# Kernel optimization log

Hardware: AMD Instinct MI355X
Metric: run time of the kernel (lower is better)

Reference implementation:

```python
import jax, jax.numpy as jnp
import numpy as np

CHUNK = 128
EPS = 1e-12


def causal_prod(q, k, v, chunk=CHUNK):
    """Chunk-parallel causal linear attention numerator and denominator.
    q,k: [B,H,S,D]; v: [B,H,S,E].
    Returns N: [B,H,S,E] = q_n . cumsum_{m<=n}(k_m v_m^T)
            D: [B,H,S]   = q_n . cumsum_{m<=n} k_m
    """
    B, H, S, D = q.shape
    E = v.shape[-1]
    nc = S // chunk
    # [nc, B, H, C, D]
    qc = q.reshape(B, H, nc, chunk, D).transpose(2, 0, 1, 3, 4)
    kc = k.reshape(B, H, nc, chunk, D).transpose(2, 0, 1, 3, 4)
    vc = v.reshape(B, H, nc, chunk, E).transpose(2, 0, 1, 3, 4)
    mask = jnp.tril(jnp.ones((chunk, chunk), dtype=bool))  # j <= i

    def step(carry, xs):
        S_state, Z_state = carry  # [B,H,D,E], [B,H,D]
        qb, kb, vb = xs           # [B,H,C,D], [B,H,C,D], [B,H,C,E]
        scores = jnp.einsum('bhid,bhjd->bhij', qb, kb)
        scores = jnp.where(mask, scores, 0.0)
        # intra-chunk causal part + inter-chunk state part
        Nb = jnp.einsum('bhij,bhje->bhie', scores, vb) \
             + jnp.einsum('bhid,bhde->bhie', qb, S_state)
        Db = scores.sum(-1) + jnp.einsum('bhid,bhd->bhi', qb, Z_state)
        S_state = S_state + jnp.einsum('bhjd,bhje->bhde', kb, vb)
        Z_state = Z_state + kb.sum(axis=2)
        return (S_state, Z_state), (Nb, Db)

    init = (jnp.zeros((B, H, D, E), q.dtype), jnp.zeros((B, H, D), q.dtype))
    _, (N, Dv) = jax.lax.scan(step, init, (qc, kc, vc))
    N = N.transpose(1, 2, 0, 3, 4).reshape(B, H, S, E)
    Dv = Dv.transpose(1, 2, 0, 3).reshape(B, H, S)
    return N, Dv


def setup_inputs() -> dict:
    key = jax.random.key(0)
    k0, k1, k2, k3, k4 = jax.random.split(key, 5)
    B, H, S, D = 2, 8, 4096, 64
    # feature-mapped q/k are positive (softmax random features) -> uniform
    q = jax.random.uniform(k0, (B, H, S, D), dtype=jnp.float32)
    k = jax.random.uniform(k1, (B, H, S, D), dtype=jnp.float32)
    q_rot = jax.random.uniform(k2, (B, H, S, D), dtype=jnp.float32)
    k_rot = jax.random.uniform(k3, (B, H, S, D), dtype=jnp.float32)
    v = jax.random.normal(k4, (B, H, S, D), dtype=jnp.float32)
    return {"q": q, "k": k, "q_rot": q_rot, "k_rot": k_rot, "v": v, "horizon": 512}


def reference(q, k, q_rot, k_rot, v, horizon):
    # causal_linear_attention with local=horizon, rotary branch active
    N1, D1 = causal_prod(q, k, v)
    N2, D2 = causal_prod(q_rot, k_rot, v)
    N = N1 + N2
    Dd = D1 + D2
    local = horizon
    # subtract contribution of keys older than the local window
    ql = q[:, :, local:]
    kl = k[:, :, :-local]
    vl = v[:, :, :-local]
    qrl = q_rot[:, :, local:]
    krl = k_rot[:, :, :-local]
    Ns1, Ds1 = causal_prod(ql, kl, vl)
    Ns2, Ds2 = causal_prod(qrl, krl, vl)
    N = N.at[:, :, local:].add(-(Ns1 + Ns2))
    Dd = Dd.at[:, :, local:].add(-(Ds1 + Ds2))
    out = N * (1.0 / (Dd + EPS))[..., None]
    return out
```

## Files before the change

### kernel.cpp

```cpp
#include <hip/hip_runtime.h>

#define S_LEN 4096
#define Dh 64
#define KC_TILE 16384
#define VT_TILE 8192

typedef __attribute__((ext_vector_type(8))) short bf16x8;
typedef __attribute__((ext_vector_type(4))) short bf16x4;
typedef __attribute__((ext_vector_type(4))) float f32x4;
typedef __attribute__((ext_vector_type(16))) float f32x16;
typedef __attribute__((ext_vector_type(4))) unsigned u32x4;

__device__ __forceinline__ short f2bf(float f) {
    union { float f; unsigned u; } c; c.f = f;
    unsigned u = c.u + 0x7FFFu + ((c.u >> 16) & 1u);
    return (short)(u >> 16);
}

__device__ __forceinline__ unsigned cvt_pk(float lo, float hi) {
    unsigned r;
    asm("v_cvt_pk_bf16_f32 %0, %1, %2" : "=v"(r) : "v"(lo), "v"(hi));
    return r;
}

__device__ __forceinline__ void pl32swap(unsigned& a, unsigned& b) {
    asm("v_permlane32_swap_b32 %0, %1" : "+v"(a), "+v"(b));
}

__global__ __launch_bounds__(256) void prepack2(
    const float* __restrict__ k, const float* __restrict__ kr,
    const float* __restrict__ v, char* __restrict__ ws,
    unsigned long long vt_base, int k_slots)
{
    const int t = blockIdx.x * 256 + threadIdx.x;
    if (t < k_slots) {
        const int bh = t >> 16;
        const int r = t & 65535;
        const int tile = r >> 10;
        const int s = r & 1023;
        const int l = s & 63;
        const int c = s >> 6;
        const int fs = c >> 1, half = c & 1;
        const int key = half * 32 + (l & 31);
        const int f0 = fs * 16 + (l >> 5) * 8;
        const size_t row = ((size_t)bh * S_LEN + tile * 64 + key) * Dh;
        const float* src = (f0 < 64) ? (k + row + f0) : (kr + row + f0 - 64);
        f32x4 a = *(const f32x4*)src;
        f32x4 b = *(const f32x4*)(src + 4);
        u32x4 w;
        w[0] = cvt_pk(a[0], a[1]); w[1] = cvt_pk(a[2], a[3]);
        w[2] = cvt_pk(b[0], b[1]); w[3] = cvt_pk(b[2], b[3]);
        *(u32x4*)(ws + (size_t)(bh * 64 + tile) * KC_TILE + s * 16) = w;
    } else {
        const int t2 = t - k_slots;
        const int bh = t2 >> 15;
        const int r = t2 & 32767;
        const int tile = r >> 9;
        const int s = r & 511;
        const int l = s & 63;
        const int c = s >> 6;
        const int kb = c >> 2, ks = (c >> 1) & 1, eh = c & 1;
        const int e = eh * 32 + (l & 31);
        const int key0 = kb * 32 + ks * 16 + (l >> 5) * 8;
        const float* src = v + ((size_t)bh * S_LEN + tile * 64 + key0) * Dh + e;
        float x0 = src[0],      x1 = src[Dh],     x2 = src[2 * Dh], x3 = src[3 * Dh];
        float x4 = src[4 * Dh], x5 = src[5 * Dh], x6 = src[6 * Dh], x7 = src[7 * Dh];
        u32x4 w;
        w[0] = cvt_pk(x0, x1); w[1] = cvt_pk(x2, x3);
        w[2] = cvt_pk(x4, x5); w[3] = cvt_pk(x6, x7);
        *(u32x4*)(ws + vt_base + (size_t)(bh * 64 + tile) * VT_TILE + s * 16) = w;
    }
}

__global__ __launch_bounds__(64, 3) void swin_attn5(
    const float* __restrict__ q, const float* __restrict__ qr,
    const char* __restrict__ ws, unsigned long long vt_base,
    const int* __restrict__ hor, float* __restrict__ out)
{
    const int W = hor[0];
    const int nwg = gridDim.x;
    const int cpx = nwg >> 3;
    const int bid = blockIdx.x;
    const int wg = (bid & 7) * cpx + (bid >> 3);
    const int bh = wg >> 7;
    const int q0 = (wg & 127) * 32;
    const size_t base = (size_t)bh * S_LEN * Dh;

    const int lane = threadIdx.x;
    const int hi = lane >> 5;
    const int l32 = lane & 31;

    __shared__ float sD[32];

    const int qg = q0 + l32;

    bf16x8 qf[8];
    {
        const float* qrow  = q  + base + (size_t)qg * Dh;
        const float* qrrow = qr + base + (size_t)qg * Dh;
        #pragma unroll
        for (int fs = 0; fs < 8; ++fs) {
            int feat = fs * 16 + hi * 8;
            const float* src = (feat < 64) ? (qrow + feat) : (qrrow + feat - 64);
            f32x4 a = *(const f32x4*)src;
            f32x4 b = *(const f32x4*)(src + 4);
            u32x4 w;
            w[0] = cvt_pk(a[0], a[1]); w[1] = cvt_pk(a[2], a[3]);
            w[2] = cvt_pk(b[0], b[1]); w[3] = cvt_pk(b[2], b[3]);
            qf[fs] = __builtin_bit_cast(bf16x8, w);
        }
    }

    f32x16 nacc0 = {};
    f32x16 nacc1 = {};
    float dsum = 0.f;

    const int lo_q = q0 - W + 1;
    const int h_lo = (lo_q <= 0) ? 0 : (lo_q >> 5);
    const int h_hi = (q0 + 31) >> 5;

    const char* Kc = ws + (size_t)(bh << 6) * KC_TILE + lane * 16;
    const char* Vt = ws + vt_base + (size_t)(bh << 6) * VT_TILE + lane * 16;

#define KADDR(H, FS) (Kc + (size_t)((H) >> 1) * KC_TILE + ((((FS) << 1) + ((H) & 1)) << 10))
#define VADDR(H, C)  (Vt + (size_t)((H) >> 1) * VT_TILE + (((((H) & 1) << 2) + (C)) << 10))

    bf16x8 kf[8];
    bf16x8 vf[4];
    #pragma unroll
    for (int fs = 0; fs < 8; ++fs) kf[fs] = *(const bf16x8*)KADDR(h_lo, fs);
    #pragma unroll
    for (int c = 0; c < 4; ++c)    vf[c] = *(const bf16x8*)VADDR(h_lo, c);

    for (int h = h_lo; h <= h_hi; ++h) {
        const int hn = (h < h_hi) ? h + 1 : h;
        const int k0h = h << 5;

        f32x16 sac = {};
        __builtin_amdgcn_s_setprio(1);
        #pragma unroll
        for (int fs = 0; fs < 8; ++fs)
            sac = __builtin_amdgcn_mfma_f32_32x32x16_bf16(kf[fs], qf[fs], sac, 0, 0, 0);
        __builtin_amdgcn_s_setprio(0);

        #pragma unroll
        for (int fs = 0; fs < 8; ++fs) kf[fs] = *(const bf16x8*)KADDR(hn, fs);

        const bool dense = (k0h + 31 <= q0) && (k0h >= q0 + 32 - W);
        if (!dense) {
            #pragma unroll
            for (int r = 0; r < 16; ++r) {
                int key = k0h + (r & 3) + 8 * (r >> 2) + 4 * hi;
                if ((unsigned)(qg - key) >= (unsigned)W) sac[r] = 0.f;
            }
        }
        #pragma unroll
        for (int r = 0; r < 16; ++r) dsum += sac[r];

        unsigned w0 = cvt_pk(sac[0],  sac[1]);
        unsigned w1 = cvt_pk(sac[2],  sac[3]);
        unsigned w2 = cvt_pk(sac[4],  sac[5]);
        unsigned w3 = cvt_pk(sac[6],  sac[7]);
        unsigned w4 = cvt_pk(sac[8],  sac[9]);
        unsigned w5 = cvt_pk(sac[10], sac[11]);
        unsigned w6 = cvt_pk(sac[12], sac[13]);
        unsigned w7 = cvt_pk(sac[14], sac[15]);
        pl32swap(w0, w2);
        pl32swap(w1, w3);
        pl32swap(w4, w6);
        pl32swap(w5, w7);
        u32x4 p0v = {w0, w1, w2, w3};
        u32x4 p1v = {w4, w5, w6, w7};
        bf16x8 pa0 = __builtin_bit_cast(bf16x8, p0v);
        bf16x8 pa1 = __builtin_bit_cast(bf16x8, p1v);

        __builtin_amdgcn_s_setprio(1);
        nacc0 = __builtin_amdgcn_mfma_f32_32x32x16_bf16(pa0, vf[0], nacc0, 0, 0, 0);
        nacc1 = __builtin_amdgcn_mfma_f32_32x32x16_bf16(pa0, vf[1], nacc1, 0, 0, 0);
        nacc0 = __builtin_amdgcn_mfma_f32_32x32x16_bf16(pa1, vf[2], nacc0, 0, 0, 0);
        nacc1 = __builtin_amdgcn_mfma_f32_32x32x16_bf16(pa1, vf[3], nacc1, 0, 0, 0);
        __builtin_amdgcn_s_setprio(0);

        #pragma unroll
        for (int c = 0; c < 4; ++c) vf[c] = *(const bf16x8*)VADDR(hn, c);
    }
#undef KADDR
#undef VADDR

    unsigned da = __builtin_bit_cast(unsigned, dsum);
    unsigned db = da;
    pl32swap(da, db);
    float dfull = __builtin_bit_cast(float, da) + __builtin_bit_cast(float, db);
    float rcq = 1.0f / (dfull + 1e-12f);
    if (lane < 32) sD[l32] = rcq;
    __syncthreads();
    float rcv[16];
    #pragma unroll
    for (int r = 0; r < 16; ++r)
        rcv[r] = sD[(r & 3) + 8 * (r >> 2) + 4 * hi];

    #pragma unroll
    for (int r = 0; r < 16; ++r) {
        const int qrow = q0 + (r & 3) + 8 * (r >> 2) + 4 * hi;
        float* o = out + base + (size_t)qrow * Dh + l32;
        o[0]  = nacc0[r] * rcv[r];
        o[32] = nacc1[r] * rcv[r];
    }
}

__global__ __launch_bounds__(256, 2) void swin_attn_fb(
    const float* __restrict__ q, const float* __restrict__ k,
    const float* __restrict__ qr, const float* __restrict__ kr,
    const float* __restrict__ v, const int* __restrict__ hor,
    float* __restrict__ out)
{
    const int W = hor[0];
    const int q0 = blockIdx.x * 128;
    const int bh = blockIdx.y;
    const size_t base = (size_t)bh * S_LEN * Dh;

    const int tid = threadIdx.x;
    const int lane = tid & 63;
    const int wv = tid >> 6;
    const int g = lane >> 4;
    const int l16 = lane & 15;

    __shared__ __align__(16) char sK[64 * 256];
    __shared__ __align__(16) char sV[64 * 128];
    __shared__ __align__(16) char sS[4][32 * 128];

    bf16x8 qf[2][4];
    #pragma unroll
    for (int rb = 0; rb < 2; ++rb) {
        int qg = q0 + wv * 32 + rb * 16 + l16;
        const float* qrow  = q  + base + (size_t)qg * Dh;
        const float* qrrow = qr + base + (size_t)qg * Dh;
        #pragma unroll
        for (int fb = 0; fb < 4; ++fb) {
            int feat = fb * 32 + g * 8;
            const float* src = (feat < 64) ? (qrow + feat) : (qrrow + (feat - 64));
            f32x4 a = *(const f32x4*)src;
            f32x4 b = *(const f32x4*)(src + 4);
            bf16x8 fr;
            #pragma unroll
            for (int j = 0; j < 4; ++j) { fr[j] = f2bf(a[j]); fr[4 + j] = f2bf(b[j]); }
            qf[rb][fb] = fr;
        }
    }

    f32x4 nacc[2][4];
    f32x4 dacc[2];
    #pragma unroll
    for (int rb = 0; rb < 2; ++rb) {
        dacc[rb] = (f32x4){0.f, 0.f, 0.f, 0.f};
        #pragma unroll
        for (int eb = 0; eb < 4; ++eb) nacc[rb][eb] = (f32x4){0.f, 0.f, 0.f, 0.f};
    }
    bf16x8 ones;
    #pragma unroll
    for (int j = 0; j < 8; ++j) ones[j] = (short)0x3F80;

    const int lo_key = q0 - (W - 1);
    const int kt_lo = (lo_key <= 0) ? 0 : (lo_key >> 6);
    const int kt_hi = (q0 + 127) >> 6;

    for (int kt = kt_lo; kt <= kt_hi; ++kt) {
        const int k0 = kt << 6;
        __syncthreads();
        #pragma unroll
        for (int i = 0; i < 4; ++i) {
            int c = tid + 256 * i;
            int row = c >> 4;
            int f0 = (c & 15) * 8;
            const float* src = (f0 < 64) ? (k  + base + (size_t)(k0 + row) * Dh + f0)
                                         : (kr + base + (size_t)(k0 + row) * Dh + (f0 - 64));
            f32x4 a = *(const f32x4*)src;
            f32x4 b = *(const f32x4*)(src + 4);
            bf16x8 w8;
            #pragma unroll
            for (int j = 0; j < 4; ++j) { w8[j] = f2bf(a[j]); w8[4 + j] = f2bf(b[j]); }
            int off = row * 256 + ((f0 * 2) ^ ((row & 7) << 4));
            *(bf16x8*)(sK + off) = w8;
        }
        #pragma unroll
        for (int i = 0; i < 4; ++i) {
            int c = tid + 256 * i;
            int e = c & 63;
            int k4 = c >> 6;
            const float* src = v + base + (size_t)(k0 + k4 * 4) * Dh + e;
            bf16x4 w4;
            w4[0] = f2bf(src[0]); w4[1] = f2bf(src[Dh]);
            w4[2] = f2bf(src[2 * Dh]); w4[3] = f2bf(src[3 * Dh]);
            int off = e * 128 + ((k4 * 8) ^ ((e & 7) << 4));
            *(bf16x4*)(sV + off) = w4;
        }
        __syncthreads();

        const bool dense = (k0 + 63 <= q0) && (k0 >= q0 + 128 - W);
        #pragma unroll
        for (int kb = 0; kb < 4; ++kb) {
            bf16x8 kf[4];
            const int key = kb * 16 + l16;
            const int rowoff = key * 256;
            const int sw = (key & 7) << 4;
            #pragma unroll
            for (int fb = 0; fb < 4; ++fb)
                kf[fb] = *(const bf16x8*)(sK + rowoff + ((fb * 64 + g * 16) ^ sw));
            #pragma unroll
            for (int rb = 0; rb < 2; ++rb) {
                f32x4 s = {0.f, 0.f, 0.f, 0.f};
                #pragma unroll
                for (int fb = 0; fb < 4; ++fb)
                    s = __builtin_amdgcn_mfma_f32_16x16x32_bf16(qf[rb][fb], kf[fb], s, 0, 0, 0);
                const int qrow0 = rb * 16 + g * 4;
                const int qg0 = q0 + wv * 32 + qrow0;
                const int mg = k0 + kb * 16 + l16;
                if (!dense) {
                    #pragma unroll
                    for (int r = 0; r < 4; ++r) {
                        unsigned d = (unsigned)(qg0 + r - mg);
                        if (d >= (unsigned)W) s[r] = 0.f;
                    }
                }
                #pragma unroll
                for (int r = 0; r < 4; ++r) {
                    int row = qrow0 + r;
                    int off = row * 128 + (((kb * 16 + l16) * 2) ^ ((row & 7) << 4));
                    *(short*)(sS[wv] + off) = f2bf(s[r]);
                }
            }
        }
        #pragma unroll
        for (int kb2 = 0; kb2 < 2; ++kb2) {
            bf16x8 af[2];
            #pragma unroll
            for (int rb = 0; rb < 2; ++rb) {
                int row = rb * 16 + l16;
                int off = row * 128 + ((kb2 * 64 + g * 16) ^ ((row & 7) << 4));
                af[rb] = *(const bf16x8*)(sS[wv] + off);
            }
            #pragma unroll
            for (int rb = 0; rb < 2; ++rb)
                dacc[rb] = __builtin_amdgcn_mfma_f32_16x16x32_bf16(af[rb], ones, dacc[rb], 0, 0, 0);
            #pragma unroll
            for (int eb = 0; eb < 4; ++eb) {
                int e = eb * 16 + l16;
                int off = e * 128 + ((kb2 * 64 + g * 16) ^ ((e & 7) << 4));
                bf16x8 bfr = *(const bf16x8*)(sV + off);
                #pragma unroll
                for (int rb = 0; rb < 2; ++rb)
                    nacc[rb][eb] = __builtin_amdgcn_mfma_f32_16x16x32_bf16(af[rb], bfr, nacc[rb][eb], 0, 0, 0);
            }
        }
    }

    #pragma unroll
    for (int rb = 0; rb < 2; ++rb) {
        f32x4 rc;
        #pragma unroll
        for (int r = 0; r < 4; ++r) rc[r] = 1.0f / (dacc[rb][r] + 1e-12f);
        const int qg0 = q0 + wv * 32 + rb * 16 + g * 4;
        #pragma unroll
        for (int eb = 0; eb < 4; ++eb) {
            #pragma unroll
            for (int r = 0; r < 4; ++r) {
                out[base + (size_t)(qg0 + r) * Dh + eb * 16 + l16] = nacc[rb][eb][r] * rc[r];
            }
        }
    }
}

extern "C" void kernel_launch(void* const* d_in, const int* in_sizes, int n_in,
                              void* d_out, int out_size, void* d_ws, size_t ws_size,
                              hipStream_t stream) {
    const float* q  = (const float*)d_in[0];
    const float* k  = (const float*)d_in[1];
    const float* qr = (const float*)d_in[2];
    const float* kr = (const float*)d_in[3];
    const float* v  = (const float*)d_in[4];
    const int* hor  = (const int*)d_in[5];
    float* out = (float*)d_out;

    const int BH = in_sizes[0] / (S_LEN * Dh);
    const unsigned long long vt_base = (unsigned long long)BH * 64 * KC_TILE;
    const unsigned long long ws_need = (unsigned long long)BH * 64 * (KC_TILE + VT_TILE);
    const int k_slots = BH * 65536;

    if (ws_size >= ws_need) {
        const int total_slots = BH * (65536 + 32768);
        hipLaunchKernelGGL(prepack2, dim3(total_slots / 256), dim3(256), 0, stream,
                           k, kr, v, (char*)d_ws, vt_base, k_slots);
        hipLaunchKernelGGL(swin_attn5, dim3(BH * 128), dim3(64), 0, stream,
                           q, qr, (const char*)d_ws, vt_base, hor, out);
    } else {
        hipLaunchKernelGGL(swin_attn_fb, dim3(S_LEN / 128, BH), dim3(256), 0, stream,
                           q, k, qr, kr, v, hor, out);
    }
}
```

Baseline: 42.91 us.

## Process two 32-query groups per wave to reuse K/V fragments

Each single-wave workgroup now handles 64 queries as two 32-row groups that share each loaded K and V fragment. Each key tile therefore feeds twice as many MFMAs, and the total K/V traffic from the workspace is roughly halved. The grid is halved and launch bounds drop to 2 waves per SIMD because the doubled Q fragments and accumulators raise register pressure. The costs are lower occupancy, fewer workgroups to hide latency with, and one extra key tile per group at the window edges.

```diff
diff --git a/kernel.cpp b/kernel.cpp
--- a/kernel.cpp
+++ b/kernel.cpp
@@ -72,7 +72,7 @@
     }
 }
 
-__global__ __launch_bounds__(64, 3) void swin_attn5(
+__global__ __launch_bounds__(64, 2) void swin_attn6(
     const float* __restrict__ q, const float* __restrict__ qr,
     const char* __restrict__ ws, unsigned long long vt_base,
     const int* __restrict__ hor, float* __restrict__ out)
@@ -82,20 +82,23 @@
     const int cpx = nwg >> 3;
     const int bid = blockIdx.x;
     const int wg = (bid & 7) * cpx + (bid >> 3);
-    const int bh = wg >> 7;
-    const int q0 = (wg & 127) * 32;
+    const int bh = wg >> 6;
+    const int q0 = (wg & 63) * 64;
     const size_t base = (size_t)bh * S_LEN * Dh;
 
     const int lane = threadIdx.x;
     const int hi = lane >> 5;
     const int l32 = lane & 31;
 
-    __shared__ float sD[32];
-
-    const int qg = q0 + l32;
-
-    bf16x8 qf[8];
-    {
+    __shared__ float sD[64];
+
+    const int qgA = q0 + l32;
+    const int qgB = q0 + 32 + l32;
+
+    bf16x8 qfA[8], qfB[8];
+    #pragma unroll
+    for (int grp = 0; grp < 2; ++grp) {
+        const int qg = grp ? qgB : qgA;
         const float* qrow  = q  + base + (size_t)qg * Dh;
         const float* qrrow = qr + base + (size_t)qg * Dh;
         #pragma unroll
@@ -107,17 +110,18 @@
             u32x4 w;
             w[0] = cvt_pk(a[0], a[1]); w[1] = cvt_pk(a[2], a[3]);
             w[2] = cvt_pk(b[0], b[1]); w[3] = cvt_pk(b[2], b[3]);
-            qf[fs] = __builtin_bit_cast(bf16x8, w);
-        }
-    }
-
-    f32x16 nacc0 = {};
-    f32x16 nacc1 = {};
-    float dsum = 0.f;
+            if (grp) qfB[fs] = __builtin_bit_cast(bf16x8, w);
+            else     qfA[fs] = __builtin_bit_cast(bf16x8, w);
+        }
+    }
+
+    f32x16 naccA0 = {}, naccA1 = {};
+    f32x16 naccB0 = {}, naccB1 = {};
+    float dsumA = 0.f, dsumB = 0.f;
 
     const int lo_q = q0 - W + 1;
     const int h_lo = (lo_q <= 0) ? 0 : (lo_q >> 5);
-    const int h_hi = (q0 + 31) >> 5;
+    const int h_hi = (q0 + 63) >> 5;
 
     const char* Kc = ws + (size_t)(bh << 6) * KC_TILE + lane * 16;
     const char* Vt = ws + vt_base + (size_t)(bh << 6) * VT_TILE + lane * 16;
@@ -136,50 +140,87 @@
         const int hn = (h < h_hi) ? h + 1 : h;
         const int k0h = h << 5;
 
-        f32x16 sac = {};
+        f32x16 sacA = {};
+        f32x16 sacB = {};
         __builtin_amdgcn_s_setprio(1);
         #pragma unroll
-        for (int fs = 0; fs < 8; ++fs)
-            sac = __builtin_amdgcn_mfma_f32_32x32x16_bf16(kf[fs], qf[fs], sac, 0, 0, 0);
+        for (int fs = 0; fs < 8; ++fs) {
+            sacA = __builtin_amdgcn_mfma_f32_32x32x16_bf16(kf[fs], qfA[fs], sacA, 0, 0, 0);
+            sacB = __builtin_amdgcn_mfma_f32_32x32x16_bf16(kf[fs], qfB[fs], sacB, 0, 0, 0);
+        }
         __builtin_amdgcn_s_setprio(0);
 
         #pragma unroll
         for (int fs = 0; fs < 8; ++fs) kf[fs] = *(const bf16x8*)KADDR(hn, fs);
 
-        const bool dense = (k0h + 31 <= q0) && (k0h >= q0 + 32 - W);
-        if (!dense) {
-            #pragma unroll
-            for (int r = 0; r < 16; ++r) {
-                int key = k0h + (r & 3) + 8 * (r >> 2) + 4 * hi;
-                if ((unsigned)(qg - key) >= (unsigned)W) sac[r] = 0.f;
-            }
-        }
-        #pragma unroll
-        for (int r = 0; r < 16; ++r) dsum += sac[r];
-
-        unsigned w0 = cvt_pk(sac[0],  sac[1]);
-        unsigned w1 = cvt_pk(sac[2],  sac[3]);
-        unsigned w2 = cvt_pk(sac[4],  sac[5]);
-        unsigned w3 = cvt_pk(sac[6],  sac[7]);
-        unsigned w4 = cvt_pk(sac[8],  sac[9]);
-        unsigned w5 = cvt_pk(sac[10], sac[11]);
-        unsigned w6 = cvt_pk(sac[12], sac[13]);
-        unsigned w7 = cvt_pk(sac[14], sac[15]);
-        pl32swap(w0, w2);
-        pl32swap(w1, w3);
-        pl32swap(w4, w6);
-        pl32swap(w5, w7);
-        u32x4 p0v = {w0, w1, w2, w3};
-        u32x4 p1v = {w4, w5, w6, w7};
-        bf16x8 pa0 = __builtin_bit_cast(bf16x8, p0v);
-        bf16x8 pa1 = __builtin_bit_cast(bf16x8, p1v);
-
-        __builtin_amdgcn_s_setprio(1);
-        nacc0 = __builtin_amdgcn_mfma_f32_32x32x16_bf16(pa0, vf[0], nacc0, 0, 0, 0);
-        nacc1 = __builtin_amdgcn_mfma_f32_32x32x16_bf16(pa0, vf[1], nacc1, 0, 0, 0);
-        nacc0 = __builtin_amdgcn_mfma_f32_32x32x16_bf16(pa1, vf[2], nacc0, 0, 0, 0);
-        nacc1 = __builtin_amdgcn_mfma_f32_32x32x16_bf16(pa1, vf[3], nacc1, 0, 0, 0);
-        __builtin_amdgcn_s_setprio(0);
+        {
+            const bool dense = (k0h + 31 <= q0) && (k0h >= q0 + 32 - W);
+            if (!dense) {
+                #pragma unroll
+                for (int r = 0; r < 16; ++r) {
+                    int key = k0h + (r & 3) + 8 * (r >> 2) + 4 * hi;
+                    if ((unsigned)(qgA - key) >= (unsigned)W) sacA[r] = 0.f;
+                }
+            }
+            #pragma unroll
+            for (int r = 0; r < 16; ++r) dsumA += sacA[r];
+
+            unsigned w0 = cvt_pk(sacA[0],  sacA[1]);
+            unsigned w1 = cvt_pk(sacA[2],  sacA[3]);
+            unsigned w2 = cvt_pk(sacA[4],  sacA[5]);
+            unsigned w3 = cvt_pk(sacA[6],  sacA[7]);
+            unsigned w4 = cvt_pk(sacA[8],  sacA[9]);
+            unsigned w5 = cvt_pk(sacA[10], sacA[11]);
+            unsigned w6 = cvt_pk(sacA[12], sacA[13]);
+            unsigned w7 = cvt_pk(sacA[14], sacA[15]);
+            pl32swap(w0, w2);  pl32swap(w1, w3);
+            pl32swap(w4, w6);  pl32swap(w5, w7);
+            u32x4 p0v = {w0, w1, w2, w3};
+            u32x4 p1v = {w4, w5, w6, w7};
+            bf16x8 pa0 = __builtin_bit_cast(bf16x8, p0v);
+            bf16x8 pa1 = __builtin_bit_cast(bf16x8, p1v);
+
+            __builtin_amdgcn_s_setprio(1);
+            naccA0 = __builtin_amdgcn_mfma_f32_32x32x16_bf16(pa0, vf[0], naccA0, 0, 0, 0);
+            naccA1 = __builtin_amdgcn_mfma_f32_32x32x16_bf16(pa0, vf[1], naccA1, 0, 0, 0);
+            naccA0 = __builtin_amdgcn_mfma_f32_32x32x16_bf16(pa1, vf[2], naccA0, 0, 0, 0);
+            naccA1 = __builtin_amdgcn_mfma_f32_32x32x16_bf16(pa1, vf[3], naccA1, 0, 0, 0);
+            __builtin_amdgcn_s_setprio(0);
+        }
+        {
+            const bool dense = (k0h + 31 <= q0 + 32) && (k0h >= q0 + 64 - W);
+            if (!dense) {
+                #pragma unroll
+                for (int r = 0; r < 16; ++r) {
+                    int key = k0h + (r & 3) + 8 * (r >> 2) + 4 * hi;
+                    if ((unsigned)(qgB - key) >= (unsigned)W) sacB[r] = 0.f;
+                }
+            }
+            #pragma unroll
+            for (int r = 0; r < 16; ++r) dsumB += sacB[r];
+
+            unsigned w0 = cvt_pk(sacB[0],  sacB[1]);
+            unsigned w1 = cvt_pk(sacB[2],  sacB[3]);
+            unsigned w2 = cvt_pk(sacB[4],  sacB[5]);
+            unsigned w3 = cvt_pk(sacB[6],  sacB[7]);
+            unsigned w4 = cvt_pk(sacB[8],  sacB[9]);
+            unsigned w5 = cvt_pk(sacB[10], sacB[11]);
+            unsigned w6 = cvt_pk(sacB[12], sacB[13]);
+            unsigned w7 = cvt_pk(sacB[14], sacB[15]);
+            pl32swap(w0, w2);  pl32swap(w1, w3);
+            pl32swap(w4, w6);  pl32swap(w5, w7);
+            u32x4 p0v = {w0, w1, w2, w3};
+            u32x4 p1v = {w4, w5, w6, w7};
+            bf16x8 pa0 = __builtin_bit_cast(bf16x8, p0v);
+            bf16x8 pa1 = __builtin_bit_cast(bf16x8, p1v);
+
+            __builtin_amdgcn_s_setprio(1);
+            naccB0 = __builtin_amdgcn_mfma_f32_32x32x16_bf16(pa0, vf[0], naccB0, 0, 0, 0);
+            naccB1 = __builtin_amdgcn_mfma_f32_32x32x16_bf16(pa0, vf[1], naccB1, 0, 0, 0);
+            naccB0 = __builtin_amdgcn_mfma_f32_32x32x16_bf16(pa1, vf[2], naccB0, 0, 0, 0);
+            naccB1 = __builtin_amdgcn_mfma_f32_32x32x16_bf16(pa1, vf[3], naccB1, 0, 0, 0);
+            __builtin_amdgcn_s_setprio(0);
+        }
 
         #pragma unroll
         for (int c = 0; c < 4; ++c) vf[c] = *(const bf16x8*)VADDR(hn, c);
@@ -187,24 +228,33 @@
 #undef KADDR
 #undef VADDR
 
-    unsigned da = __builtin_bit_cast(unsigned, dsum);
-    unsigned db = da;
-    pl32swap(da, db);
-    float dfull = __builtin_bit_cast(float, da) + __builtin_bit_cast(float, db);
-    float rcq = 1.0f / (dfull + 1e-12f);
-    if (lane < 32) sD[l32] = rcq;
+    {
+        unsigned da = __builtin_bit_cast(unsigned, dsumA);
+        unsigned db = da;
+        pl32swap(da, db);
+        float dfull = __builtin_bit_cast(float, da) + __builtin_bit_cast(float, db);
+        if (lane < 32) sD[l32] = 1.0f / (dfull + 1e-12f);
+    }
+    {
+        unsigned da = __builtin_bit_cast(unsigned, dsumB);
+        unsigned db = da;
+        pl32swap(da, db);
+        float dfull = __builtin_bit_cast(float, da) + __builtin_bit_cast(float, db);
+        if (lane < 32) sD[32 + l32] = 1.0f / (dfull + 1e-12f);
+    }
     __syncthreads();
-    float rcv[16];
-    #pragma unroll
-    for (int r = 0; r < 16; ++r)
-        rcv[r] = sD[(r & 3) + 8 * (r >> 2) + 4 * hi];
 
     #pragma unroll
     for (int r = 0; r < 16; ++r) {
-        const int qrow = q0 + (r & 3) + 8 * (r >> 2) + 4 * hi;
-        float* o = out + base + (size_t)qrow * Dh + l32;
-        o[0]  = nacc0[r] * rcv[r];
-        o[32] = nacc1[r] * rcv[r];
+        const int crow = (r & 3) + 8 * (r >> 2) + 4 * hi;
+        const float rcA = sD[crow];
+        const float rcB = sD[32 + crow];
+        float* oA = out + base + (size_t)(q0 + crow) * Dh + l32;
+        float* oB = out + base + (size_t)(q0 + 32 + crow) * Dh + l32;
+        oA[0]  = naccA0[r] * rcA;
+        oA[32] = naccA1[r] * rcA;
+        oB[0]  = naccB0[r] * rcB;
+        oB[32] = naccB1[r] * rcB;
     }
 }
 
@@ -390,7 +440,7 @@
         const int total_slots = BH * (65536 + 32768);
         hipLaunchKernelGGL(prepack2, dim3(total_slots / 256), dim3(256), 0, stream,
                            k, kr, v, (char*)d_ws, vt_base, k_slots);
-        hipLaunchKernelGGL(swin_attn5, dim3(BH * 128), dim3(64), 0, stream,
+        hipLaunchKernelGGL(swin_attn6, dim3(BH * 64), dim3(64), 0, stream,
                            q, qr, (const char*)d_ws, vt_base, hor, out);
     } else {
         hipLaunchKernelGGL(swin_attn_fb, dim3(S_LEN / 128, BH), dim3(256), 0, stream,
```

Result: slower. 43.88 us (+2.3%).

## Split each query tile's key range across two waves with an LDS reduction

Applied to the files above, without the earlier changes.

The attention kernel now launches 4-wave workgroups covering 64 queries. Each pair of waves shares one 32-query tile and splits that tile's key blocks into two halves. The second wave writes its partial numerator and denominator to shared memory, and the first wave adds them, normalises and stores the output. This halves each wave's serial MFMA/load chain and doubles the number of waves in flight, at the cost of an LDS round-trip, a block barrier, and some idle waves during the epilogue.

```diff
diff --git a/kernel.cpp b/kernel.cpp
--- a/kernel.cpp
+++ b/kernel.cpp
@@ -72,7 +72,7 @@
     }
 }
 
-__global__ __launch_bounds__(64, 3) void swin_attn5(
+__global__ __launch_bounds__(256, 3) void swin_attn7(
     const float* __restrict__ q, const float* __restrict__ qr,
     const char* __restrict__ ws, unsigned long long vt_base,
     const int* __restrict__ hor, float* __restrict__ out)
@@ -82,17 +82,24 @@
     const int cpx = nwg >> 3;
     const int bid = blockIdx.x;
     const int wg = (bid & 7) * cpx + (bid >> 3);
-    const int bh = wg >> 7;
-    const int q0 = (wg & 127) * 32;
+    const int bh = wg >> 6;
+    const int q0 = (wg & 63) * 64;
     const size_t base = (size_t)bh * S_LEN * Dh;
 
-    const int lane = threadIdx.x;
+    const int tid = threadIdx.x;
+    const int lane = tid & 63;
+    const int wv = tid >> 6;
+    const int qtile = wv >> 1;
+    const int seg = wv & 1;
     const int hi = lane >> 5;
     const int l32 = lane & 31;
 
-    __shared__ float sD[32];
-
-    const int qg = q0 + l32;
+    __shared__ __align__(16) char sN[2][8192];
+    __shared__ float sDs[2][64];
+    __shared__ float sRc[2][32];
+
+    const int q0w = q0 + qtile * 32;
+    const int qg = q0w + l32;
 
     bf16x8 qf[8];
     {
@@ -115,9 +122,14 @@
     f32x16 nacc1 = {};
     float dsum = 0.f;
 
-    const int lo_q = q0 - W + 1;
+    const int lo_q = q0w - W + 1;
     const int h_lo = (lo_q <= 0) ? 0 : (lo_q >> 5);
-    const int h_hi = (q0 + 31) >> 5;
+    const int h_hi = (q0w + 31) >> 5;
+    const int nh = h_hi - h_lo + 1;
+    const int nh0 = (nh + 1) >> 1;
+    const int hs = seg ? (h_lo + nh0) : h_lo;
+    const int he = seg ? h_hi : (h_lo + nh0 - 1);
+    const int hs_c = (hs > he) ? he : hs;
 
     const char* Kc = ws + (size_t)(bh << 6) * KC_TILE + lane * 16;
     const char* Vt = ws + vt_base + (size_t)(bh << 6) * VT_TILE + lane * 16;
@@ -128,12 +140,12 @@
     bf16x8 kf[8];
     bf16x8 vf[4];
     #pragma unroll
-    for (int fs = 0; fs < 8; ++fs) kf[fs] = *(const bf16x8*)KADDR(h_lo, fs);
-    #pragma unroll
-    for (int c = 0; c < 4; ++c)    vf[c] = *(const bf16x8*)VADDR(h_lo, c);
-
-    for (int h = h_lo; h <= h_hi; ++h) {
-        const int hn = (h < h_hi) ? h + 1 : h;
+    for (int fs = 0; fs < 8; ++fs) kf[fs] = *(const bf16x8*)KADDR(hs_c, fs);
+    #pragma unroll
+    for (int c = 0; c < 4; ++c)    vf[c] = *(const bf16x8*)VADDR(hs_c, c);
+
+    for (int h = hs; h <= he; ++h) {
+        const int hn = (h < he) ? h + 1 : h;
         const int k0h = h << 5;
 
         f32x16 sac = {};
@@ -146,7 +158,7 @@
         #pragma unroll
         for (int fs = 0; fs < 8; ++fs) kf[fs] = *(const bf16x8*)KADDR(hn, fs);
 
-        const bool dense = (k0h + 31 <= q0) && (k0h >= q0 + 32 - W);
+        const bool dense = (k0h + 31 <= q0w) && (k0h >= q0w + 32 - W);
         if (!dense) {
             #pragma unroll
             for (int r = 0; r < 16; ++r) {
@@ -187,24 +199,51 @@
 #undef KADDR
 #undef VADDR
 
-    unsigned da = __builtin_bit_cast(unsigned, dsum);
-    unsigned db = da;
-    pl32swap(da, db);
-    float dfull = __builtin_bit_cast(float, da) + __builtin_bit_cast(float, db);
-    float rcq = 1.0f / (dfull + 1e-12f);
-    if (lane < 32) sD[l32] = rcq;
+    if (seg == 1) {
+        char* dst = sN[qtile] + lane * 16;
+        #pragma unroll
+        for (int cc = 0; cc < 4; ++cc) {
+            f32x4 v4 = {nacc0[cc * 4], nacc0[cc * 4 + 1], nacc0[cc * 4 + 2], nacc0[cc * 4 + 3]};
+            *(f32x4*)(dst + cc * 1024) = v4;
+        }
+        #pragma unroll
+        for (int cc = 0; cc < 4; ++cc) {
+            f32x4 v4 = {nacc1[cc * 4], nacc1[cc * 4 + 1], nacc1[cc * 4 + 2], nacc1[cc * 4 + 3]};
+            *(f32x4*)(dst + 4096 + cc * 1024) = v4;
+        }
+        sDs[qtile][lane] = dsum;
+    }
     __syncthreads();
-    float rcv[16];
-    #pragma unroll
-    for (int r = 0; r < 16; ++r)
-        rcv[r] = sD[(r & 3) + 8 * (r >> 2) + 4 * hi];
-
-    #pragma unroll
-    for (int r = 0; r < 16; ++r) {
-        const int qrow = q0 + (r & 3) + 8 * (r >> 2) + 4 * hi;
-        float* o = out + base + (size_t)qrow * Dh + l32;
-        o[0]  = nacc0[r] * rcv[r];
-        o[32] = nacc1[r] * rcv[r];
+    if (seg == 0) {
+        const char* src = sN[qtile] + lane * 16;
+        #pragma unroll
+        for (int cc = 0; cc < 4; ++cc) {
+            f32x4 v4 = *(const f32x4*)(src + cc * 1024);
+            nacc0[cc * 4] += v4[0]; nacc0[cc * 4 + 1] += v4[1];
+            nacc0[cc * 4 + 2] += v4[2]; nacc0[cc * 4 + 3] += v4[3];
+        }
+        #pragma unroll
+        for (int cc = 0; cc < 4; ++cc) {
+            f32x4 v4 = *(const f32x4*)(src + 4096 + cc * 1024);
+            nacc1[cc * 4] += v4[0]; nacc1[cc * 4 + 1] += v4[1];
+            nacc1[cc * 4 + 2] += v4[2]; nacc1[cc * 4 + 3] += v4[3];
+        }
+        dsum += sDs[qtile][lane];
+
+        unsigned da = __builtin_bit_cast(unsigned, dsum);
+        unsigned db = da;
+        pl32swap(da, db);
+        float dfull = __builtin_bit_cast(float, da) + __builtin_bit_cast(float, db);
+        if (lane < 32) sRc[qtile][l32] = 1.0f / (dfull + 1e-12f);
+
+        #pragma unroll
+        for (int r = 0; r < 16; ++r) {
+            const int crow = (r & 3) + 8 * (r >> 2) + 4 * hi;
+            const float rc = sRc[qtile][crow];
+            float* o = out + base + (size_t)(q0w + crow) * Dh + l32;
+            o[0]  = nacc0[r] * rc;
+            o[32] = nacc1[r] * rc;
+        }
     }
 }
 
@@ -390,7 +429,7 @@
         const int total_slots = BH * (65536 + 32768);
         hipLaunchKernelGGL(prepack2, dim3(total_slots / 256), dim3(256), 0, stream,
                            k, kr, v, (char*)d_ws, vt_base, k_slots);
-        hipLaunchKernelGGL(swin_attn5, dim3(BH * 128), dim3(64), 0, stream,
+        hipLaunchKernelGGL(swin_attn7, dim3(BH * 64), dim3(256), 0, stream,
                            q, qr, (const char*)d_ws, vt_base, hor, out);
     } else {
         hipLaunchKernelGGL(swin_attn_fb, dim3(S_LEN / 128, BH), dim3(256), 0, stream,
```

Result: slower. 44.80 us (+4.4%).
